# Kernel optimization log

Hardware: AMD Instinct MI355X
Metric: run time of the kernel (lower is better)

## Reference

```python
import jax, jax.numpy as jnp
import numpy as np

EMBED = 1024
HEADS = 16
HEAD_DIM = EMBED // HEADS


def setup_inputs() -> dict:
    key = jax.random.key(0)
    k1, k2, k3, k4, k5 = jax.random.split(key, 5)
    N, S = 2, 2048
    values = jax.random.normal(k1, (N, S, EMBED), dtype=jnp.float32)
    keys = jax.random.normal(k2, (N, S, EMBED), dtype=jnp.float32)
    query = jax.random.normal(k3, (N, S, EMBED), dtype=jnp.float32)
    mask = jnp.ones((N, 1, S, S), dtype=jnp.int32)
    # fc_out: Linear(heads*head_dim, embed_size) with bias; torch stores W as [out, in]
    W_out = jax.random.normal(k4, (EMBED, EMBED), dtype=jnp.float32) / np.sqrt(EMBED)
    b_out = jax.random.normal(k5, (EMBED,), dtype=jnp.float32) * 0.01
    return {"values": values, "keys": keys, "query": query, "mask": mask,
            "W_out": W_out, "b_out": b_out}


def reference(values, keys, query, mask, W_out, b_out):
    N, S, E = query.shape
    H, D = HEADS, HEAD_DIM
    # NOTE: source module never applies its q/k/v Linear layers (bug preserved).
    v = values.reshape(N, S, H, D)
    k = keys.reshape(N, S, H, D)
    q = query.reshape(N, S, H, D)
    energy = jnp.einsum('nqhd,nkhd->nhqk', q, k)  # [N,H,S,S]
    energy = jnp.where(mask == 0, jnp.float32(-1e20), energy)
    # non-standard scale: sqrt(embed_size), faithful to source
    attn = jax.nn.softmax(energy / jnp.sqrt(jnp.float32(E)), axis=3)
    out = jnp.einsum('nhql,nlhd->nqhd', attn, v).reshape(N, S, H * D)
    return out @ W_out.T + b_out
```

## Files before the change

kernel.cpp:

```cpp
#include <hip/hip_runtime.h>
#include <stdint.h>

#define S_LEN 2048
#define EMB 1024
#define NHEADS 16
#define HD 64
#define LOG2E 1.4426950408889634f
#define NROWS 65536

typedef __bf16 bf16x8 __attribute__((ext_vector_type(8)));
typedef float f32x4 __attribute__((ext_vector_type(4)));
typedef unsigned short u16;

#define MFMA16(a, b, c) __builtin_amdgcn_mfma_f32_16x16x32_bf16(a, b, c, 0, 0, 0)
#define GLOAD_LDS16(gp, lp)                                        \
  __builtin_amdgcn_global_load_lds(                                \
      (const __attribute__((address_space(1))) unsigned int*)(gp), \
      (__attribute__((address_space(3))) unsigned int*)(lp), 16, 0, 0)

__device__ __forceinline__ u16 bf16r(float x) {
  union { float f; unsigned int u; } c; c.f = x;
  unsigned int u = c.u + 0x7fffu + ((c.u >> 16) & 1u);
  return (u16)(u >> 16);
}

__device__ __forceinline__ unsigned int cvt_pk_bf16(float lo, float hi) {
  unsigned int r;
  asm("v_cvt_pk_bf16_f32 %0, %1, %2" : "=v"(r) : "v"(lo), "v"(hi));
  return r;
}

__device__ __forceinline__ float fexp2(float x) {
  float r;
  asm("v_exp_f32 %0, %1" : "=v"(r) : "v"(x));
  return r;
}

__device__ __forceinline__ float fmax3(float a, float b, float c) {
  float r;
  asm("v_max3_f32 %0, %1, %2, %3" : "=v"(r) : "v"(a), "v"(b), "v"(c));
  return r;
}

__device__ __forceinline__ int kperm(int k) {
  int kb = (k >> 4) & 3, g = (k >> 2) & 3, r = k & 3;
  return (kb >> 1) * 32 + g * 8 + (kb & 1) * 4 + r;
}

__global__ __launch_bounds__(256) void prep_kernel(
    const float* __restrict__ values, const float* __restrict__ keys,
    const float* __restrict__ W, const int* __restrict__ mask,
    u16* __restrict__ vt, u16* __restrict__ kb, u16* __restrict__ wb,
    unsigned char* __restrict__ fl2) {
  __shared__ u16 tile[64][65];
  __shared__ int s_ok[4];
  int b = blockIdx.x;
  int t = threadIdx.x;
  if (b < 1024) {
    int st = b & 31, h = (b >> 5) & 15, n = b >> 9;
    int s0 = st * 64;
    int d = t & 63, r4 = t >> 6;
#pragma unroll
    for (int i = 0; i < 16; ++i) {
      int s = r4 + i * 4;
      float x = values[(size_t)(n * S_LEN + s0 + s) * EMB + h * HD + d];
      tile[s][d] = bf16r(x);
    }
    __syncthreads();
    int sp = s0 + kperm(d);
#pragma unroll
    for (int i = 0; i < 16; ++i) {
      int dd = r4 + i * 4;
      vt[(size_t)((n * NHEADS + h) * HD + dd) * S_LEN + sp] = tile[d][dd];
    }
  } else if (b < 2048) {
    int idx = (b - 1024) * 256 + t;
    const float4* in4 = (const float4*)keys;
    ushort4* out4 = (ushort4*)kb;
#pragma unroll
    for (int j = 0; j < 4; ++j) {
      float4 v = in4[idx + j * 262144];
      ushort4 o;
      o.x = bf16r(v.x); o.y = bf16r(v.y); o.z = bf16r(v.z); o.w = bf16r(v.w);
      out4[idx + j * 262144] = o;
    }
  } else if (b < 2304) {
    int idx = (b - 2048) * 256 + t;
    const float4* in4 = (const float4*)W;
    ushort4* out4 = (ushort4*)wb;
#pragma unroll
    for (int j = 0; j < 4; ++j) {
      float4 v = in4[idx + j * 65536];
      ushort4 o;
      o.x = bf16r(v.x); o.y = bf16r(v.y); o.z = bf16r(v.z); o.w = bf16r(v.w);
      out4[idx + j * 65536] = o;
    }
  } else {
    int idx = b - 2304;
    int kt = idx & 31, qt = (idx >> 5) & 15, n = idx >> 9;
    int qr = t >> 1, c8 = t & 1;
    const int4* mp = (const int4*)(mask + (size_t)n * S_LEN * S_LEN +
                                   (size_t)(qt * 128 + qr) * S_LEN + kt * 64) + c8 * 8;
    int ok = 1;
#pragma unroll
    for (int i = 0; i < 8; ++i) {
      int4 m = mp[i];
      ok &= (m.x != 0) & (m.y != 0) & (m.z != 0) & (m.w != 0);
    }
    ok = __all(ok);
    if ((t & 63) == 0) s_ok[t >> 6] = ok;
    __syncthreads();
    if (t == 0) fl2[idx] = (unsigned char)(s_ok[0] & s_ok[1] & s_ok[2] & s_ok[3]);
  }
}

__global__ __launch_bounds__(256, 4) void attn_kernel(
    const float* __restrict__ query, const u16* __restrict__ kbuf,
    const u16* __restrict__ vt, const int* __restrict__ mask,
    const unsigned char* __restrict__ fl2, float* __restrict__ po,
    float2* __restrict__ ml) {
  __shared__ __align__(16) unsigned char kl[2][8192];
  __shared__ __align__(16) unsigned char vl[2][8192];

  int b = blockIdx.x;
  b = (b & 7) * 128 + (b >> 3);
  int qt = b & 15, half = (b >> 4) & 1, h = (b >> 5) & 15, n = b >> 9;
  int t = threadIdx.x, w = t >> 6, l = t & 63, l16 = l & 15, g = l >> 4;
  int q0 = qt * 128 + w * 32;
  int kt0 = half * 16;

  const float QS = 0.03125f * LOG2E;
  bf16x8 aq[2][2];
#pragma unroll
  for (int u = 0; u < 2; ++u)
#pragma unroll
    for (int hh = 0; hh < 2; ++hh) {
      const float* qp = query + (size_t)(n * S_LEN + q0 + u * 16 + l16) * EMB +
                        h * HD + hh * 32 + g * 8;
      float4 f0 = *(const float4*)qp;
      float4 f1 = *(const float4*)(qp + 4);
      union { bf16x8 v; unsigned int u32[4]; } qq;
      qq.u32[0] = cvt_pk_bf16(f0.x * QS, f0.y * QS);
      qq.u32[1] = cvt_pk_bf16(f0.z * QS, f0.w * QS);
      qq.u32[2] = cvt_pk_bf16(f1.x * QS, f1.y * QS);
      qq.u32[3] = cvt_pk_bf16(f1.z * QS, f1.w * QS);
      aq[u][hh] = qq.v;
    }

  union { bf16x8 v; unsigned int u32[4]; } one_i;
  one_i.u32[0] = 0x3F803F80u; one_i.u32[1] = 0x3F803F80u;
  one_i.u32[2] = 0x3F803F80u; one_i.u32[3] = 0x3F803F80u;
  bf16x8 ones = one_i.v;

  f32x4 zero4 = {0.f, 0.f, 0.f, 0.f};
  f32x4 acc[2][4];
  float lrun[2] = {0.f, 0.f}, mrun[2] = {0.f, 0.f};
#pragma unroll
  for (int u = 0; u < 2; ++u)
#pragma unroll
    for (int db = 0; db < 4; ++db) acc[u][db] = zero4;

  int row_s = t >> 3, cc = t & 7;
  int sc = cc ^ (row_s & 7);
  const u16* gk0 = kbuf + (size_t)(n * S_LEN + row_s) * EMB + h * HD + sc * 8;
  const u16* gv0 = vt + (size_t)((n * NHEADS + h) * HD + row_s) * S_LEN + sc * 8;

  auto stage = [&](int kt, int nb) {
    const u16* gk = gk0 + (size_t)kt * 64 * EMB;
    const u16* gv = gv0 + kt * 64;
    GLOAD_LDS16(gk, kl[nb] + (w * 64) * 16);
    GLOAD_LDS16(gk + 32 * EMB, kl[nb] + (256 + w * 64) * 16);
    GLOAD_LDS16(gv, vl[nb] + (w * 64) * 16);
    GLOAD_LDS16(gv + 32 * S_LEN, vl[nb] + (256 + w * 64) * 16);
  };

  stage(kt0, 0);
  __syncthreads();

  for (int kt = kt0; kt < kt0 + 16; ++kt) {
    int cur = kt & 1;
    if (kt + 1 < kt0 + 16) stage(kt + 1, cur ^ 1);
    const unsigned char* kc = kl[cur];
    const unsigned char* vc = vl[cur];

    f32x4 sf[2][4];
    __builtin_amdgcn_s_setprio(1);
#pragma unroll
    for (int kb = 0; kb < 4; ++kb) {
      int row = kb * 16 + l16;
      const unsigned char* kr = kc + row * 128;
      int sw = (row & 7) << 4;
      bf16x8 bk0 = *(const bf16x8*)(kr + ((g * 16) ^ sw));
      bf16x8 bk1 = *(const bf16x8*)(kr + ((64 + g * 16) ^ sw));
#pragma unroll
      for (int u = 0; u < 2; ++u) {
        f32x4 z = zero4;
        z = MFMA16(bk0, aq[u][0], z);
        z = MFMA16(bk1, aq[u][1], z);
        sf[u][kb] = z;
      }
    }
    __builtin_amdgcn_s_setprio(0);

    unsigned char fflag = fl2[((n * 16 + qt) * 32) + kt];
    if (!fflag) {
#pragma unroll
      for (int u = 0; u < 2; ++u) {
        const int* mrow = mask + (size_t)n * S_LEN * S_LEN +
                          (size_t)(q0 + u * 16 + l16) * S_LEN + kt * 64 + g * 4;
#pragma unroll
        for (int kb = 0; kb < 4; ++kb) {
          int4 mm = *(const int4*)(mrow + kb * 16);
          if (mm.x == 0) sf[u][kb][0] = -100.f;
          if (mm.y == 0) sf[u][kb][1] = -100.f;
          if (mm.z == 0) sf[u][kb][2] = -100.f;
          if (mm.w == 0) sf[u][kb][3] = -100.f;
        }
      }
    }

    bf16x8 pa[2][2];
#pragma unroll
    for (int u = 0; u < 2; ++u) {
      float a0 = fmax3(sf[u][0][0], sf[u][0][1], sf[u][0][2]);
      float a1 = fmax3(sf[u][0][3], sf[u][1][0], sf[u][1][1]);
      float a2 = fmax3(sf[u][1][2], sf[u][1][3], sf[u][2][0]);
      float a3 = fmax3(sf[u][2][1], sf[u][2][2], sf[u][2][3]);
      float a4 = fmax3(sf[u][3][0], sf[u][3][1], sf[u][3][2]);
      float lmax = fmaxf(fmax3(a0, a1, a2), fmax3(a3, a4, sf[u][3][3]));
      if (!__all(lmax <= mrun[u] + 8.f)) {
        float rmax = fmaxf(lmax, __shfl_xor(lmax, 16));
        rmax = fmaxf(rmax, __shfl_xor(rmax, 32));
        float Mn = fmaxf(mrun[u], rmax);
        float corr = fexp2(mrun[u] - Mn);
        mrun[u] = Mn;
        lrun[u] *= corr;
#pragma unroll
        for (int r = 0; r < 4; ++r) {
          float ca = __shfl(corr, (l & 48) + (g << 2) + r);
#pragma unroll
          for (int db = 0; db < 4; ++db) acc[u][db][r] *= ca;
        }
      }
      float p[4][4];
      if (__all(mrun[u] == 0.f)) {
#pragma unroll
        for (int kb = 0; kb < 4; ++kb)
#pragma unroll
          for (int r = 0; r < 4; ++r) p[kb][r] = fexp2(sf[u][kb][r]);
      } else {
#pragma unroll
        for (int kb = 0; kb < 4; ++kb)
#pragma unroll
          for (int r = 0; r < 4; ++r) p[kb][r] = fexp2(sf[u][kb][r] - mrun[u]);
      }
#pragma unroll
      for (int hh = 0; hh < 2; ++hh) {
        union { bf16x8 v; unsigned int u32[4]; } pp;
        pp.u32[0] = cvt_pk_bf16(p[2 * hh][0], p[2 * hh][1]);
        pp.u32[1] = cvt_pk_bf16(p[2 * hh][2], p[2 * hh][3]);
        pp.u32[2] = cvt_pk_bf16(p[2 * hh + 1][0], p[2 * hh + 1][1]);
        pp.u32[3] = cvt_pk_bf16(p[2 * hh + 1][2], p[2 * hh + 1][3]);
        pa[u][hh] = pp.v;
      }
      f32x4 z = zero4;
      z = MFMA16(pa[u][0], ones, z);
      z = MFMA16(pa[u][1], ones, z);
      float z01 = (l16 & 1) ? z[1] : z[0];
      float z23 = (l16 & 1) ? z[3] : z[2];
      float zsel = (l16 & 2) ? z23 : z01;
      lrun[u] += __shfl(zsel, ((l16 >> 2) << 4) + (l16 & 3));
    }

    __builtin_amdgcn_s_setprio(1);
#pragma unroll
    for (int hh = 0; hh < 2; ++hh)
#pragma unroll
      for (int db = 0; db < 4; ++db) {
        int d = db * 16 + l16;
        bf16x8 bv = *(const bf16x8*)(vc + d * 128 + ((hh * 64 + g * 16) ^ ((d & 7) << 4)));
        acc[0][db] = MFMA16(pa[0][hh], bv, acc[0][db]);
        acc[1][db] = MFMA16(pa[1][hh], bv, acc[1][db]);
      }
    __builtin_amdgcn_s_setprio(0);

    __syncthreads();
  }

  size_t rowbase = (size_t)(n * NHEADS + h) * S_LEN + q0;
#pragma unroll
  for (int u = 0; u < 2; ++u) {
    if (g == 0) {
      float2 v; v.x = mrun[u]; v.y = lrun[u];
      ml[(size_t)half * NROWS + rowbase + u * 16 + l16] = v;
    }
#pragma unroll
    for (int db = 0; db < 4; ++db)
#pragma unroll
      for (int r = 0; r < 4; ++r) {
        size_t rq = rowbase + u * 16 + (g << 2) + r;
        po[((size_t)half * NROWS + rq) * HD + db * 16 + l16] = acc[u][db][r];
      }
  }
}

__global__ __launch_bounds__(256) void combine_kernel(
    const float* __restrict__ po, const float2* __restrict__ ml,
    u16* __restrict__ ob) {
  int idx = blockIdx.x * 256 + threadIdx.x;
  int row = idx >> 4, d4 = idx & 15;
  float2 a = ml[row], b = ml[NROWS + row];
  float m = fmaxf(a.x, b.x);
  float c0 = fexp2(a.x - m), c1 = fexp2(b.x - m);
  float rinv = 1.f / (a.y * c0 + b.y * c1);
  c0 *= rinv; c1 *= rinv;
  float4 o0 = ((const float4*)po)[(size_t)row * 16 + d4];
  float4 o1 = ((const float4*)po)[(size_t)NROWS * 16 + (size_t)row * 16 + d4];
  ushort4 o;
  o.x = bf16r(o0.x * c0 + o1.x * c1);
  o.y = bf16r(o0.y * c0 + o1.y * c1);
  o.z = bf16r(o0.z * c0 + o1.z * c1);
  o.w = bf16r(o0.w * c0 + o1.w * c1);
  int n = row >> 15, h = (row >> 11) & 15, q = row & 2047;
  *(ushort4*)(ob + (size_t)(n * S_LEN + q) * EMB + h * HD + d4 * 4) = o;
}

__global__ __launch_bounds__(256) void proj_kernel(
    const u16* __restrict__ A, const u16* __restrict__ Bt,
    const float* __restrict__ bias, float* __restrict__ C) {
  __shared__ __align__(16) unsigned char al[2][16384];
  __shared__ __align__(16) unsigned char bl[2][8192];
  int bm = blockIdx.x, bn = blockIdx.y;
  int t = threadIdx.x, w = t >> 6, l = t & 63;
  int l16 = l & 15, g = l >> 4;
  f32x4 zero4 = {0.f, 0.f, 0.f, 0.f};
  f32x4 acc[2][4];
#pragma unroll
  for (int mi = 0; mi < 2; ++mi)
#pragma unroll
    for (int nj = 0; nj < 4; ++nj) acc[mi][nj] = zero4;
  int row_s = t >> 3, cc = t & 7;
  int sc = cc ^ (row_s & 7);
  const u16* ga0 = A + (size_t)(bm * 128 + row_s) * EMB + sc * 8;
  const u16* gb0 = Bt + (size_t)(bn * 64 + row_s) * EMB + sc * 8;

  auto stage = [&](int ks, int nb) {
#pragma unroll
    for (int i = 0; i < 4; ++i)
      GLOAD_LDS16(ga0 + (size_t)i * 32 * EMB + ks * 64, al[nb] + (i * 256 + w * 64) * 16);
#pragma unroll
    for (int i = 0; i < 2; ++i)
      GLOAD_LDS16(gb0 + (size_t)i * 32 * EMB + ks * 64, bl[nb] + (i * 256 + w * 64) * 16);
  };

  stage(0, 0);
  __syncthreads();

  for (int ks = 0; ks < 16; ++ks) {
    int cur = ks & 1;
    if (ks + 1 < 16) stage(ks + 1, cur ^ 1);
    __builtin_amdgcn_s_setprio(1);
#pragma unroll
    for (int hh = 0; hh < 2; ++hh) {
      bf16x8 af[2], bfr[4];
#pragma unroll
      for (int mi = 0; mi < 2; ++mi) {
        int row = w * 32 + mi * 16 + l16;
        af[mi] = *(const bf16x8*)(al[cur] + row * 128 + ((hh * 64 + g * 16) ^ ((row & 7) << 4)));
      }
#pragma unroll
      for (int nj = 0; nj < 4; ++nj) {
        int row = nj * 16 + l16;
        bfr[nj] = *(const bf16x8*)(bl[cur] + row * 128 + ((hh * 64 + g * 16) ^ ((row & 7) << 4)));
      }
#pragma unroll
      for (int mi = 0; mi < 2; ++mi)
#pragma unroll
        for (int nj = 0; nj < 4; ++nj) acc[mi][nj] = MFMA16(af[mi], bfr[nj], acc[mi][nj]);
    }
    __builtin_amdgcn_s_setprio(0);
    __syncthreads();
  }
#pragma unroll
  for (int nj = 0; nj < 4; ++nj) {
    int j = bn * 64 + nj * 16 + l16;
    float bj = bias[j];
#pragma unroll
    for (int mi = 0; mi < 2; ++mi) {
      int i0 = bm * 128 + w * 32 + mi * 16 + g * 4;
#pragma unroll
      for (int r = 0; r < 4; ++r) C[(size_t)(i0 + r) * EMB + j] = acc[mi][nj][r] + bj;
    }
  }
}

extern "C" void kernel_launch(void* const* d_in, const int* in_sizes, int n_in,
                              void* d_out, int out_size, void* d_ws, size_t ws_size,
                              hipStream_t stream) {
  const float* values = (const float*)d_in[0];
  const float* keys = (const float*)d_in[1];
  const float* query = (const float*)d_in[2];
  const int* mask = (const int*)d_in[3];
  const float* W = (const float*)d_in[4];
  const float* bias = (const float*)d_in[5];
  float* out = (float*)d_out;

  u16* kb = (u16*)d_ws;
  u16* vt = kb + 4194304;
  u16* ob = vt + 4194304;
  u16* wb = ob + 4194304;
  unsigned char* fl2 = (unsigned char*)(wb + 1048576);
  float* po = (float*)(fl2 + 65536);
  float2* ml = (float2*)(po + 2 * (size_t)NROWS * HD);

  prep_kernel<<<3328, 256, 0, stream>>>(values, keys, W, mask, vt, kb, wb, fl2);
  attn_kernel<<<1024, 256, 0, stream>>>(query, kb, vt, mask, fl2, po, ml);
  combine_kernel<<<4096, 256, 0, stream>>>(po, ml, ob);
  proj_kernel<<<dim3(32, 16), 256, 0, stream>>>(ob, wb, bias, out);
}
```

Baseline: 90.89 us.

## Store split-K partial outputs in bf16, unroll double-buffer loops, bump proj occupancy

Attention partial outputs are rounded to bf16 before being written, which halves the traffic to and from the partial buffer. The combine kernel now reads 8 bf16 values per thread and packs its output with v_cvt_pk_bf16, so it launches half as many blocks. The attention and projection main loops are manually unrolled by two with fixed LDS buffer indices, and proj_kernel gets a launch bound asking for 3 blocks per CU. Rounding the partials to bf16 adds one extra rounding step before the final combine.

```diff
diff --git a/kernel.cpp b/kernel.cpp
--- a/kernel.cpp
+++ b/kernel.cpp
@@ -40,6 +40,13 @@
   float r;
   asm("v_max3_f32 %0, %1, %2, %3" : "=v"(r) : "v"(a), "v"(b), "v"(c));
   return r;
+}
+
+__device__ __forceinline__ float bf_lo(unsigned int v) {
+  union { unsigned int u; float f; } c; c.u = v << 16; return c.f;
+}
+__device__ __forceinline__ float bf_hi(unsigned int v) {
+  union { unsigned int u; float f; } c; c.u = v & 0xffff0000u; return c.f;
 }
 
 __device__ __forceinline__ int kperm(int k) {
@@ -117,7 +124,7 @@
 __global__ __launch_bounds__(256, 4) void attn_kernel(
     const float* __restrict__ query, const u16* __restrict__ kbuf,
     const u16* __restrict__ vt, const int* __restrict__ mask,
-    const unsigned char* __restrict__ fl2, float* __restrict__ po,
+    const unsigned char* __restrict__ fl2, u16* __restrict__ po,
     float2* __restrict__ ml) {
   __shared__ __align__(16) unsigned char kl[2][8192];
   __shared__ __align__(16) unsigned char vl[2][8192];
@@ -174,15 +181,7 @@
     GLOAD_LDS16(gv + 32 * S_LEN, vl[nb] + (256 + w * 64) * 16);
   };
 
-  stage(kt0, 0);
-  __syncthreads();
-
-  for (int kt = kt0; kt < kt0 + 16; ++kt) {
-    int cur = kt & 1;
-    if (kt + 1 < kt0 + 16) stage(kt + 1, cur ^ 1);
-    const unsigned char* kc = kl[cur];
-    const unsigned char* vc = vl[cur];
-
+  auto body = [&](int kt, const unsigned char* kc, const unsigned char* vc) {
     f32x4 sf[2][4];
     __builtin_amdgcn_s_setprio(1);
 #pragma unroll
@@ -283,7 +282,18 @@
         acc[1][db] = MFMA16(pa[1][hh], bv, acc[1][db]);
       }
     __builtin_amdgcn_s_setprio(0);
-
+  };
+
+  stage(kt0, 0);
+  __syncthreads();
+
+#pragma unroll 1
+  for (int kt = kt0; kt < kt0 + 16; kt += 2) {
+    stage(kt + 1, 1);
+    body(kt, kl[0], vl[0]);
+    __syncthreads();
+    if (kt + 2 < kt0 + 16) stage(kt + 2, 0);
+    body(kt + 1, kl[1], vl[1]);
     __syncthreads();
   }
 
@@ -299,33 +309,37 @@
 #pragma unroll
       for (int r = 0; r < 4; ++r) {
         size_t rq = rowbase + u * 16 + (g << 2) + r;
-        po[((size_t)half * NROWS + rq) * HD + db * 16 + l16] = acc[u][db][r];
+        po[((size_t)half * NROWS + rq) * HD + db * 16 + l16] = bf16r(acc[u][db][r]);
       }
   }
 }
 
 __global__ __launch_bounds__(256) void combine_kernel(
-    const float* __restrict__ po, const float2* __restrict__ ml,
+    const u16* __restrict__ po, const float2* __restrict__ ml,
     u16* __restrict__ ob) {
   int idx = blockIdx.x * 256 + threadIdx.x;
-  int row = idx >> 4, d4 = idx & 15;
+  int row = idx >> 3, d8 = idx & 7;
   float2 a = ml[row], b = ml[NROWS + row];
   float m = fmaxf(a.x, b.x);
   float c0 = fexp2(a.x - m), c1 = fexp2(b.x - m);
   float rinv = 1.f / (a.y * c0 + b.y * c1);
   c0 *= rinv; c1 *= rinv;
-  float4 o0 = ((const float4*)po)[(size_t)row * 16 + d4];
-  float4 o1 = ((const float4*)po)[(size_t)NROWS * 16 + (size_t)row * 16 + d4];
-  ushort4 o;
-  o.x = bf16r(o0.x * c0 + o1.x * c1);
-  o.y = bf16r(o0.y * c0 + o1.y * c1);
-  o.z = bf16r(o0.z * c0 + o1.z * c1);
-  o.w = bf16r(o0.w * c0 + o1.w * c1);
+  uint4 p0 = *(const uint4*)(po + (size_t)row * HD + d8 * 8);
+  uint4 p1 = *(const uint4*)(po + ((size_t)NROWS + row) * HD + d8 * 8);
+  uint4 o;
+  o.x = cvt_pk_bf16(bf_lo(p0.x) * c0 + bf_lo(p1.x) * c1,
+                    bf_hi(p0.x) * c0 + bf_hi(p1.x) * c1);
+  o.y = cvt_pk_bf16(bf_lo(p0.y) * c0 + bf_lo(p1.y) * c1,
+                    bf_hi(p0.y) * c0 + bf_hi(p1.y) * c1);
+  o.z = cvt_pk_bf16(bf_lo(p0.z) * c0 + bf_lo(p1.z) * c1,
+                    bf_hi(p0.z) * c0 + bf_hi(p1.z) * c1);
+  o.w = cvt_pk_bf16(bf_lo(p0.w) * c0 + bf_lo(p1.w) * c1,
+                    bf_hi(p0.w) * c0 + bf_hi(p1.w) * c1);
   int n = row >> 15, h = (row >> 11) & 15, q = row & 2047;
-  *(ushort4*)(ob + (size_t)(n * S_LEN + q) * EMB + h * HD + d4 * 4) = o;
-}
-
-__global__ __launch_bounds__(256) void proj_kernel(
+  *(uint4*)(ob + (size_t)(n * S_LEN + q) * EMB + h * HD + d8 * 8) = o;
+}
+
+__global__ __launch_bounds__(256, 3) void proj_kernel(
     const u16* __restrict__ A, const u16* __restrict__ Bt,
     const float* __restrict__ bias, float* __restrict__ C) {
   __shared__ __align__(16) unsigned char al[2][16384];
@@ -353,32 +367,39 @@
       GLOAD_LDS16(gb0 + (size_t)i * 32 * EMB + ks * 64, bl[nb] + (i * 256 + w * 64) * 16);
   };
 
+  auto body = [&](const unsigned char* ac, const unsigned char* bc) {
+    __builtin_amdgcn_s_setprio(1);
+#pragma unroll
+    for (int hh = 0; hh < 2; ++hh) {
+      bf16x8 af[2], bfr[4];
+#pragma unroll
+      for (int mi = 0; mi < 2; ++mi) {
+        int row = w * 32 + mi * 16 + l16;
+        af[mi] = *(const bf16x8*)(ac + row * 128 + ((hh * 64 + g * 16) ^ ((row & 7) << 4)));
+      }
+#pragma unroll
+      for (int nj = 0; nj < 4; ++nj) {
+        int row = nj * 16 + l16;
+        bfr[nj] = *(const bf16x8*)(bc + row * 128 + ((hh * 64 + g * 16) ^ ((row & 7) << 4)));
+      }
+#pragma unroll
+      for (int mi = 0; mi < 2; ++mi)
+#pragma unroll
+        for (int nj = 0; nj < 4; ++nj) acc[mi][nj] = MFMA16(af[mi], bfr[nj], acc[mi][nj]);
+    }
+    __builtin_amdgcn_s_setprio(0);
+  };
+
   stage(0, 0);
   __syncthreads();
 
-  for (int ks = 0; ks < 16; ++ks) {
-    int cur = ks & 1;
-    if (ks + 1 < 16) stage(ks + 1, cur ^ 1);
-    __builtin_amdgcn_s_setprio(1);
-#pragma unroll
-    for (int hh = 0; hh < 2; ++hh) {
-      bf16x8 af[2], bfr[4];
-#pragma unroll
-      for (int mi = 0; mi < 2; ++mi) {
-        int row = w * 32 + mi * 16 + l16;
-        af[mi] = *(const bf16x8*)(al[cur] + row * 128 + ((hh * 64 + g * 16) ^ ((row & 7) << 4)));
-      }
-#pragma unroll
-      for (int nj = 0; nj < 4; ++nj) {
-        int row = nj * 16 + l16;
-        bfr[nj] = *(const bf16x8*)(bl[cur] + row * 128 + ((hh * 64 + g * 16) ^ ((row & 7) << 4)));
-      }
-#pragma unroll
-      for (int mi = 0; mi < 2; ++mi)
-#pragma unroll
-        for (int nj = 0; nj < 4; ++nj) acc[mi][nj] = MFMA16(af[mi], bfr[nj], acc[mi][nj]);
-    }
-    __builtin_amdgcn_s_setprio(0);
+#pragma unroll 1
+  for (int ks = 0; ks < 16; ks += 2) {
+    stage(ks + 1, 1);
+    body(al[0], bl[0]);
+    __syncthreads();
+    if (ks + 2 < 16) stage(ks + 2, 0);
+    body(al[1], bl[1]);
     __syncthreads();
   }
 #pragma unroll
@@ -410,11 +431,11 @@
   u16* ob = vt + 4194304;
   u16* wb = ob + 4194304;
   unsigned char* fl2 = (unsigned char*)(wb + 1048576);
-  float* po = (float*)(fl2 + 65536);
+  u16* po = (u16*)(fl2 + 65536);
   float2* ml = (float2*)(po + 2 * (size_t)NROWS * HD);
 
   prep_kernel<<<3328, 256, 0, stream>>>(values, keys, W, mask, vt, kb, wb, fl2);
   attn_kernel<<<1024, 256, 0, stream>>>(query, kb, vt, mask, fl2, po, ml);
-  combine_kernel<<<4096, 256, 0, stream>>>(po, ml, ob);
+  combine_kernel<<<2048, 256, 0, stream>>>(po, ml, ob);
   proj_kernel<<<dim3(32, 16), 256, 0, stream>>>(ob, wb, bias, out);
 }
```

Result: faster. 87.58 us, median of 2 (-3.6%).
